# Performance work log

Hardware: AMD Instinct MI355X
Metric: run time of the kernel (lower is better)

The kernel has to match this reference:

```python
import jax, jax.numpy as jnp
import numpy as np

EMBED = 1024
DMODEL = 1024
NHEAD = 16
HEAD = DMODEL // NHEAD  # 64
EPS = 1e-5


def layer_norm(x, g, b):
    mu = jnp.mean(x, axis=-1, keepdims=True)
    var = jnp.var(x, axis=-1, keepdims=True)
    return (x - mu) / jnp.sqrt(var + EPS) * g + b


def setup_inputs() -> dict:
    key = jax.random.key(0)
    ks = jax.random.split(key, 16)
    s = 0.02
    B, T = 2, 2048
    return {
        "x": jax.random.normal(ks[0], (B, T, EMBED), jnp.float32),
        "wq": jax.random.normal(ks[1], (NHEAD, EMBED, HEAD), jnp.float32) * s,
        "bq": jnp.zeros((NHEAD, HEAD), jnp.float32),
        "wk": jax.random.normal(ks[2], (NHEAD, EMBED, HEAD), jnp.float32) * s,
        "bk": jnp.zeros((NHEAD, HEAD), jnp.float32),
        "wv": jax.random.normal(ks[3], (NHEAD, EMBED, HEAD), jnp.float32) * s,
        "bv": jnp.zeros((NHEAD, HEAD), jnp.float32),
        "ln1_g": jnp.ones((EMBED,), jnp.float32),
        "ln1_b": jnp.zeros((EMBED,), jnp.float32),
        "ln2_g": jnp.ones((DMODEL,), jnp.float32),
        "ln2_b": jnp.zeros((DMODEL,), jnp.float32),
        "w1": jax.random.normal(ks[4], (DMODEL, 4 * DMODEL), jnp.float32) * s,
        "b1": jnp.zeros((4 * DMODEL,), jnp.float32),
        "w2": jax.random.normal(ks[5], (4 * DMODEL, EMBED), jnp.float32) * s,
        "b2": jnp.zeros((EMBED,), jnp.float32),
    }


def reference(x, wq, bq, wk, bk, wv, bv, ln1_g, ln1_b, ln2_g, ln2_b, w1, b1, w2, b2):
    B, T, C = x.shape
    h = layer_norm(x, ln1_g, ln1_b)  # note: residual uses the normalized x (as in source)
    # per-head projections, vectorized over heads: [B,H,T,D]
    q = jnp.einsum('btc,hcd->bhtd', h, wq) + bq[None, :, None, :]
    k = jnp.einsum('btc,hcd->bhtd', h, wk) + bk[None, :, None, :]
    v = jnp.einsum('btc,hcd->bhtd', h, wv) + bv[None, :, None, :]
    scores = jnp.einsum('bhtd,bhsd->bhts', q, k) / jnp.sqrt(jnp.float32(HEAD))
    causal = jnp.tril(jnp.ones((T, T), bool))
    scores = jnp.where(causal[None, None], scores, jnp.finfo(scores.dtype).min)
    wei = jax.nn.softmax(scores, axis=-1)
    attn = jnp.einsum('bhts,bhsd->bhtd', wei, v)
    attn = attn.transpose(0, 2, 1, 3).reshape(B, T, NHEAD * HEAD)  # concat heads
    y = h + attn
    z = layer_norm(y, ln2_g, ln2_b)
    ff = jax.nn.relu(z @ w1 + b1) @ w2 + b2
    return z + ff
```

## Files before the change

### kernel.cpp

```cpp
#include <hip/hip_runtime.h>
#include <hip/hip_bf16.h>
#include <cstdint>
#include <cstddef>

typedef __attribute__((ext_vector_type(8))) short bf16x8;
typedef __attribute__((ext_vector_type(4))) float f32x4;
typedef __attribute__((ext_vector_type(4))) short short4v;
typedef __attribute__((ext_vector_type(2))) unsigned int uint2v;

__device__ inline void gload_lds16(const void* g, void* l) {
  __builtin_amdgcn_global_load_lds((const __attribute__((address_space(1))) void*)g,
                                   (__attribute__((address_space(3))) void*)l, 16, 0, 0);
}

__device__ inline float exp2_fast(float x) {
  float r;
  asm volatile("v_exp_f32 %0, %1" : "=v"(r) : "v"(x));
  return r;
}

__device__ inline unsigned int cvt_pk_bf16(float lo, float hi) {
  unsigned int r;
  asm volatile("v_cvt_pk_bf16_f32 %0, %1, %2" : "=v"(r) : "v"(lo), "v"(hi));
  return r;
}

__device__ inline float bf2f(short s) {
  return __uint_as_float(((unsigned int)(unsigned short)s) << 16);
}

__global__ void transpose_pack(const float* __restrict__ src, __hip_bfloat16* __restrict__ dst,
                               int R, int C, int ldDst, long zSrcStride, int zDstRow)
{
  __shared__ float tile[64][65];
  src += (size_t)blockIdx.z * zSrcStride;
  const int r0 = blockIdx.y * 64, c0 = blockIdx.x * 64;
  const int t = threadIdx.x;
#pragma unroll
  for (int i = 0; i < 16; ++i) {
    int idx = i * 256 + t;
    int r = idx >> 6, c = idx & 63;
    tile[r][c] = src[(size_t)(r0 + r) * C + c0 + c];
  }
  __syncthreads();
  const int drow0 = blockIdx.z * zDstRow + c0;
#pragma unroll
  for (int i = 0; i < 16; ++i) {
    int idx = i * 256 + t;
    int cc = idx >> 6, rr = idx & 63;
    dst[(size_t)(drow0 + cc) * ldDst + r0 + rr] = __float2bfloat16(tile[rr][cc]);
  }
}

__global__ void transpose_qkv(const float* __restrict__ wq, const float* __restrict__ wk,
                              const float* __restrict__ wv, __hip_bfloat16* __restrict__ dst)
{
  __shared__ float tile[64][65];
  const int z = blockIdx.z;
  const int seg = z >> 4, h = z & 15;
  const float* src = (seg == 0) ? wq : (seg == 1) ? wk : wv;
  src += (size_t)h * 65536;
  const int r0 = blockIdx.y * 64;
  const int t = threadIdx.x;
#pragma unroll
  for (int i = 0; i < 16; ++i) {
    int idx = i * 256 + t;
    int r = idx >> 6, c = idx & 63;
    tile[r][c] = src[(size_t)(r0 + r) * 64 + c];
  }
  __syncthreads();
  const int drow0 = seg * 1024 + h * 64;
#pragma unroll
  for (int i = 0; i < 16; ++i) {
    int idx = i * 256 + t;
    int cc = idx >> 6, rr = idx & 63;
    dst[(size_t)(drow0 + cc) * 1024 + r0 + rr] = __float2bfloat16(tile[rr][cc]);
  }
}

__global__ void ln_fused(const float* __restrict__ x,
                         const float* __restrict__ g, const float* __restrict__ bta,
                         float* __restrict__ of32, __hip_bfloat16* __restrict__ obf)
{
  const int row = blockIdx.x;
  const int t = threadIdx.x;
  float4 v = ((const float4*)(x + (size_t)row * 1024))[t];
  float s = v.x + v.y + v.z + v.w;
  float ss = v.x * v.x + v.y * v.y + v.z * v.z + v.w * v.w;
#pragma unroll
  for (int off = 1; off < 64; off <<= 1) {
    s += __shfl_xor(s, off);
    ss += __shfl_xor(ss, off);
  }
  __shared__ float sb[4], ssb[4];
  const int w = t >> 6, lane = t & 63;
  if (lane == 0) { sb[w] = s; ssb[w] = ss; }
  __syncthreads();
  s = sb[0] + sb[1] + sb[2] + sb[3];
  ss = ssb[0] + ssb[1] + ssb[2] + ssb[3];
  const float mu = s * (1.f / 1024.f);
  const float var = ss * (1.f / 1024.f) - mu * mu;
  const float rstd = rsqrtf(var + 1e-5f);
  float4 gv = ((const float4*)g)[t];
  float4 bv = ((const float4*)bta)[t];
  float4 o;
  o.x = (v.x - mu) * rstd * gv.x + bv.x;
  o.y = (v.y - mu) * rstd * gv.y + bv.y;
  o.z = (v.z - mu) * rstd * gv.z + bv.z;
  o.w = (v.w - mu) * rstd * gv.w + bv.w;
  ((float4*)(of32 + (size_t)row * 1024))[t] = o;
  __hip_bfloat16 hb[4] = { __float2bfloat16(o.x), __float2bfloat16(o.y),
                           __float2bfloat16(o.z), __float2bfloat16(o.w) };
  *(short4v*)(obf + (size_t)row * 1024 + t * 4) = *(const short4v*)hb;
}

__global__ void ln2_merge_fused(const float* __restrict__ hres,
                                const __hip_bfloat16* __restrict__ Opart,
                                const float* __restrict__ Lpart,
                                const float* __restrict__ g, const float* __restrict__ bta,
                                float* __restrict__ of32, __hip_bfloat16* __restrict__ obf)
{
  const int row = blockIdx.x;
  const int b = row >> 11, tt = row & 2047;
  const int qblk = tt >> 7, qloc = tt & 127;
  const int nch = (qblk >> 2) + 1;
  const int t = threadIdx.x;
  const int hd = t >> 4;
  const int d0 = (t & 15) * 4;
  const int base = ((b * 16 + hd) * 16 + qblk) << 2;

  float4 v = ((const float4*)(hres + (size_t)row * 1024))[t];
  float l = 0.f;
  float o0 = 0.f, o1 = 0.f, o2 = 0.f, o3 = 0.f;
  for (int ch = 0; ch < nch; ++ch) {
    l += Lpart[(size_t)(base + ch) * 128 + qloc];
    short4v o4 = *(const short4v*)(Opart + (size_t)(base + ch) * 8192 + qloc * 64 + d0);
    o0 += bf2f(o4[0]); o1 += bf2f(o4[1]); o2 += bf2f(o4[2]); o3 += bf2f(o4[3]);
  }
  const float inv = 1.f / l;
  v.x += o0 * inv; v.y += o1 * inv; v.z += o2 * inv; v.w += o3 * inv;

  float s = v.x + v.y + v.z + v.w;
  float ss = v.x * v.x + v.y * v.y + v.z * v.z + v.w * v.w;
#pragma unroll
  for (int off = 1; off < 64; off <<= 1) {
    s += __shfl_xor(s, off);
    ss += __shfl_xor(ss, off);
  }
  __shared__ float sb[4], ssb[4];
  const int w = t >> 6, lane = t & 63;
  if (lane == 0) { sb[w] = s; ssb[w] = ss; }
  __syncthreads();
  s = sb[0] + sb[1] + sb[2] + sb[3];
  ss = ssb[0] + ssb[1] + ssb[2] + ssb[3];
  const float mu = s * (1.f / 1024.f);
  const float var = ss * (1.f / 1024.f) - mu * mu;
  const float rstd = rsqrtf(var + 1e-5f);
  float4 gv = ((const float4*)g)[t];
  float4 bv = ((const float4*)bta)[t];
  float4 o;
  o.x = (v.x - mu) * rstd * gv.x + bv.x;
  o.y = (v.y - mu) * rstd * gv.y + bv.y;
  o.z = (v.z - mu) * rstd * gv.z + bv.z;
  o.w = (v.w - mu) * rstd * gv.w + bv.w;
  ((float4*)(of32 + (size_t)row * 1024))[t] = o;
  __hip_bfloat16 hb[4] = { __float2bfloat16(o.x), __float2bfloat16(o.y),
                           __float2bfloat16(o.z), __float2bfloat16(o.w) };
  *(short4v*)(obf + (size_t)row * 1024 + t * 4) = *(const short4v*)hb;
}

template<int EPI>
__global__ __launch_bounds__(512, 2) void gemm_bt(
    const __hip_bfloat16* __restrict__ A, const __hip_bfloat16* __restrict__ Bt,
    int N, int Kf, int kLen,
    const float* __restrict__ bias,
    const float* __restrict__ bq, const float* __restrict__ bk, const float* __restrict__ bv,
    __hip_bfloat16* __restrict__ oq, __hip_bfloat16* __restrict__ ok, __hip_bfloat16* __restrict__ ovt,
    __hip_bfloat16* __restrict__ obf,
    __hip_bfloat16* __restrict__ opart0, __hip_bfloat16* __restrict__ opart1,
    __hip_bfloat16* __restrict__ opart2, __hip_bfloat16* __restrict__ opart3)
{
  __shared__ short As[2][128 * 32];
  __shared__ short Bs[2][256 * 32];
  const int t = threadIdx.x;
  const int lane = t & 63;
  const int w = t >> 6;
  const int wm = w >> 2, wn = w & 3;
  const int l15 = lane & 15, lg = lane >> 4;

  const int nwg = (int)(gridDim.x * gridDim.y);
  int wgid = (int)blockIdx.y * (int)gridDim.x + (int)blockIdx.x;
  wgid = (wgid & 7) * (nwg >> 3) + (wgid >> 3);
  const int bx = wgid % (int)gridDim.x;
  const int by = wgid / (int)gridDim.x;
  const int m0 = by * 128;
  const int n0 = bx * 256;
  const int kBase = (EPI == 2) ? (int)blockIdx.z * kLen : 0;
  const int kEnd0 = kBase + kLen;
  const int kEnd = (kEnd0 > Kf) ? Kf : kEnd0;

  f32x4 acc[4][4];
#pragma unroll
  for (int i = 0; i < 4; ++i)
#pragma unroll
    for (int j = 0; j < 4; ++j)
#pragma unroll
      for (int e = 0; e < 4; ++e) acc[i][j][e] = 0.f;

  auto STAGE = [&](int buf, int kk0) {
    {
      const int r = t >> 2, cc = t & 3;
      const int kk = (cc ^ ((r >> 1) & 3)) * 8;
      gload_lds16(A + (size_t)(m0 + r) * Kf + kk0 + kk, (char*)As + buf * 8192 + t * 16);
    }
#pragma unroll
    for (int i = 0; i < 2; ++i) {
      const int c = t + 512 * i;
      const int r = c >> 2, cc = c & 3;
      const int kk = (cc ^ ((r >> 1) & 3)) * 8;
      gload_lds16(Bt + (size_t)(n0 + r) * Kf + kk0 + kk, (char*)Bs + buf * 16384 + c * 16);
    }
  };

  STAGE(0, kBase);
  int buf = 0;
  for (int k0 = kBase; k0 < kEnd; k0 += 32) {
    const int knext = (k0 + 32 < kEnd) ? k0 + 32 : k0;
    STAGE(buf ^ 1, knext);
    asm volatile("s_waitcnt vmcnt(3)" ::: "memory");
    __builtin_amdgcn_s_barrier();
    asm volatile("" ::: "memory");

    bf16x8 af[4], bfr[4];
#pragma unroll
    for (int fm = 0; fm < 4; ++fm) {
      const int r = wm * 64 + fm * 16 + l15;
      const int kc = lg ^ ((r >> 1) & 3);
      af[fm] = *(const bf16x8*)&As[buf][r * 32 + kc * 8];
    }
#pragma unroll
    for (int fn = 0; fn < 4; ++fn) {
      const int r = wn * 64 + fn * 16 + l15;
      const int kc = lg ^ ((r >> 1) & 3);
      bfr[fn] = *(const bf16x8*)&Bs[buf][r * 32 + kc * 8];
    }
#pragma unroll
    for (int fm = 0; fm < 4; ++fm)
#pragma unroll
      for (int fn = 0; fn < 4; ++fn)
        acc[fm][fn] = __builtin_amdgcn_mfma_f32_16x16x32_bf16(af[fm], bfr[fn], acc[fm][fn], 0, 0, 0);

    asm volatile("" ::: "memory");
    __builtin_amdgcn_s_barrier();
    buf ^= 1;
  }

#pragma unroll
  for (int fm = 0; fm < 4; ++fm) {
    const int mbase = m0 + wm * 64 + fm * 16 + lg * 4;
#pragma unroll
    for (int fn = 0; fn < 4; ++fn) {
      const int n = n0 + wn * 64 + fn * 16 + l15;
      if (EPI == 0) {
        const int seg = n >> 10;
        const int cn = n & 1023;
        const int h = cn >> 6, d = cn & 63;
        const float* bp = (seg == 0) ? bq : (seg == 1) ? bk : bv;
        const float bias_v = bp[cn];
#pragma unroll
        for (int rg = 0; rg < 4; ++rg) {
          const int m = mbase + rg;
          const int b = m >> 11, tt = m & 2047;
          const size_t bh = (size_t)(b * 16 + h);
          const float val = acc[fm][fn][rg] + bias_v;
          if (seg == 0)      oq[(bh * 2048 + tt) * 64 + d] = __float2bfloat16(val);
          else if (seg == 1) ok[(bh * 2048 + tt) * 64 + d] = __float2bfloat16(val);
          else               ovt[(bh * 64 + d) * 2048 + tt] = __float2bfloat16(val);
        }
      } else if (EPI == 1) {
        const float bias_v = bias[n];
#pragma unroll
        for (int rg = 0; rg < 4; ++rg) {
          const int m = mbase + rg;
          float val = acc[fm][fn][rg] + bias_v;
          val = fmaxf(val, 0.f);
          obf[(size_t)m * N + n] = __float2bfloat16(val);
        }
      } else {
        __hip_bfloat16* op = (blockIdx.z == 0) ? opart0 : (blockIdx.z == 1) ? opart1
                           : (blockIdx.z == 2) ? opart2 : opart3;
#pragma unroll
        for (int rg = 0; rg < 4; ++rg) {
          const int m = mbase + rg;
          op[(size_t)m * 1024 + n] = __float2bfloat16(acc[fm][fn][rg]);
        }
      }
    }
  }
}

__global__ void ffn2_merge(const __hip_bfloat16* __restrict__ p0, const __hip_bfloat16* __restrict__ p1,
                           const __hip_bfloat16* __restrict__ p2, const __hip_bfloat16* __restrict__ p3,
                           const float* __restrict__ z, const float* __restrict__ b2,
                           float* __restrict__ out)
{
  const size_t i = ((size_t)blockIdx.x * 256 + threadIdx.x) * 4;
  const float4 c = *(const float4*)(z + i);
  const float4 bb = *(const float4*)(b2 + (i & 1023));
  float o0 = c.x + bb.x, o1 = c.y + bb.y, o2 = c.z + bb.z, o3 = c.w + bb.w;
  short4v a0 = *(const short4v*)(p0 + i);
  short4v a1 = *(const short4v*)(p1 + i);
  short4v a2 = *(const short4v*)(p2 + i);
  short4v a3 = *(const short4v*)(p3 + i);
  o0 += bf2f(a0[0]) + bf2f(a1[0]) + bf2f(a2[0]) + bf2f(a3[0]);
  o1 += bf2f(a0[1]) + bf2f(a1[1]) + bf2f(a2[1]) + bf2f(a3[1]);
  o2 += bf2f(a0[2]) + bf2f(a1[2]) + bf2f(a2[2]) + bf2f(a3[2]);
  o3 += bf2f(a0[3]) + bf2f(a1[3]) + bf2f(a2[3]) + bf2f(a3[3]);
  float4 o; o.x = o0; o.y = o1; o.z = o2; o.w = o3;
  *(float4*)(out + i) = o;
}

__global__ __launch_bounds__(256, 3) void flash_attn(
    const __hip_bfloat16* __restrict__ Q, const __hip_bfloat16* __restrict__ Kb,
    const __hip_bfloat16* __restrict__ Vt,
    __hip_bfloat16* __restrict__ Opart, float* __restrict__ Lpart)
{
  __shared__ short Ks[2][64 * 64];
  __shared__ short Vs[2][64 * 64];
  __shared__ short P2[4][32 * 72];
  const int t = threadIdx.x;
  const int lane = t & 63, w = t >> 6;
  const int l15 = lane & 15, lg = lane >> 4;
  const int chunk = blockIdx.x, bh = blockIdx.z;
  const int qblk = 15 - (int)blockIdx.y;
  const int q0 = qblk * 128;
  const int s_base = chunk * 512;
  if (s_base > q0 + 127) return;
  const int s_hi = (s_base + 512 < q0 + 128) ? s_base + 512 : q0 + 128;
  const int ntiles = (s_hi - s_base) >> 6;
  const int qw = q0 + w * 32;

  const __hip_bfloat16* Qbh = Q + (size_t)bh * 2048 * 64;
  const __hip_bfloat16* Kbh = Kb + (size_t)bh * 2048 * 64;
  const __hip_bfloat16* Vbh = Vt + (size_t)bh * 64 * 2048;

  bf16x8 qf[2][2];
#pragma unroll
  for (int fm = 0; fm < 2; ++fm)
#pragma unroll
    for (int kc = 0; kc < 2; ++kc)
      qf[fm][kc] = *(const bf16x8*)(Qbh + (size_t)(qw + fm * 16 + l15) * 64 + kc * 32 + lg * 8);

  const int srow = (w << 4) + (lane >> 3);
  const int schunk = ((lane & 7) ^ (lane >> 3)) * 8;

  auto STAGE = [&](int bufi, int s0) {
#pragma unroll
    for (int i = 0; i < 2; ++i) {
      const int r = srow + i * 8;
      const int dst = bufi * 8192 + w * 2048 + i * 1024 + lane * 16;
      gload_lds16(Kbh + (size_t)(s0 + r) * 64 + schunk, (char*)Ks + dst);
      gload_lds16(Vbh + (size_t)r * 2048 + s0 + schunk, (char*)Vs + dst);
    }
  };

  f32x4 o_acc[2][4];
  float lpart[2] = {0.f, 0.f};
#pragma unroll
  for (int fm = 0; fm < 2; ++fm)
#pragma unroll
    for (int fd = 0; fd < 4; ++fd)
#pragma unroll
      for (int e = 0; e < 4; ++e) o_acc[fm][fd][e] = 0.f;

  const float C = 0.18033688011112042f;

  STAGE(0, s_base);
  int cur = 0;
  for (int ti = 0; ti < ntiles; ++ti) {
    const int s0 = s_base + ti * 64;
    const int nxt = (ti + 1 < ntiles) ? s0 + 64 : s0;
    STAGE(cur ^ 1, nxt);
    asm volatile("s_waitcnt vmcnt(4)" ::: "memory");
    __builtin_amdgcn_s_barrier();
    asm volatile("" ::: "memory");

    if (s0 <= qw + 31) {
      f32x4 s_acc[2][4];
#pragma unroll
      for (int fm = 0; fm < 2; ++fm)
#pragma unroll
        for (int fn = 0; fn < 4; ++fn)
#pragma unroll
          for (int e = 0; e < 4; ++e) s_acc[fm][fn][e] = 0.f;
      __builtin_amdgcn_s_setprio(1);
#pragma unroll
      for (int kc = 0; kc < 2; ++kc)
#pragma unroll
        for (int fn = 0; fn < 4; ++fn) {
          const int r = fn * 16 + l15;
          bf16x8 kf = *(const bf16x8*)&Ks[cur][r * 64 + ((((kc << 2) | lg) ^ (l15 & 7)) << 3)];
          s_acc[0][fn] = __builtin_amdgcn_mfma_f32_16x16x32_bf16(kf, qf[0][kc], s_acc[0][fn], 0, 0, 0);
          s_acc[1][fn] = __builtin_amdgcn_mfma_f32_16x16x32_bf16(kf, qf[1][kc], s_acc[1][fn], 0, 0, 0);
        }
      __builtin_amdgcn_s_setprio(0);

      const bool needmask = (s0 + 63 > qw);
      float pr[2][4][4];
#pragma unroll
      for (int fm = 0; fm < 2; ++fm) {
        const int qv = qw + fm * 16 + l15;
#pragma unroll
        for (int fn = 0; fn < 4; ++fn)
#pragma unroll
          for (int rg = 0; rg < 4; ++rg) {
            float p = exp2_fast(s_acc[fm][fn][rg] * C);
            if (needmask) {
              const int sg = s0 + fn * 16 + lg * 4 + rg;
              p = (sg <= qv) ? p : 0.f;
            }
            pr[fm][fn][rg] = p;
            lpart[fm] += p;
          }
      }

#pragma unroll
      for (int fm = 0; fm < 2; ++fm)
#pragma unroll
        for (int fn = 0; fn < 4; ++fn) {
          uint2v u;
          u.x = cvt_pk_bf16(pr[fm][fn][0], pr[fm][fn][1]);
          u.y = cvt_pk_bf16(pr[fm][fn][2], pr[fm][fn][3]);
          *(uint2v*)&P2[w][(fm * 16 + l15) * 72 + fn * 16 + lg * 4] = u;
        }

      __builtin_amdgcn_s_setprio(1);
#pragma unroll
      for (int kc = 0; kc < 2; ++kc) {
        bf16x8 pf0 = *(const bf16x8*)&P2[w][(l15) * 72 + kc * 32 + lg * 8];
        bf16x8 pf1 = *(const bf16x8*)&P2[w][(16 + l15) * 72 + kc * 32 + lg * 8];
#pragma unroll
        for (int fd = 0; fd < 4; ++fd) {
          const int r = fd * 16 + l15;
          bf16x8 vf = *(const bf16x8*)&Vs[cur][r * 64 + ((((kc << 2) | lg) ^ (l15 & 7)) << 3)];
          o_acc[0][fd] = __builtin_amdgcn_mfma_f32_16x16x32_bf16(vf, pf0, o_acc[0][fd], 0, 0, 0);
          o_acc[1][fd] = __builtin_amdgcn_mfma_f32_16x16x32_bf16(vf, pf1, o_acc[1][fd], 0, 0, 0);
        }
      }
      __builtin_amdgcn_s_setprio(0);
    }

    asm volatile("" ::: "memory");
    __builtin_amdgcn_s_barrier();
    cur ^= 1;
  }

  const int pslot = ((bh * 16 + qblk) << 2) + chunk;
  __hip_bfloat16* op = Opart + (size_t)pslot * 8192;
#pragma unroll
  for (int fm = 0; fm < 2; ++fm) {
    float l = lpart[fm];
    l += __shfl_xor(l, 16);
    l += __shfl_xor(l, 32);
    const int qloc = w * 32 + fm * 16 + l15;
    if (lg == 0) Lpart[pslot * 128 + qloc] = l;
#pragma unroll
    for (int fd = 0; fd < 4; ++fd) {
      uint2v u;
      u.x = cvt_pk_bf16(o_acc[fm][fd][0], o_acc[fm][fd][1]);
      u.y = cvt_pk_bf16(o_acc[fm][fd][2], o_acc[fm][fd][3]);
      *(uint2v*)(op + (size_t)qloc * 64 + fd * 16 + lg * 4) = u;
    }
  }
}

extern "C" void kernel_launch(void* const* d_in, const int* in_sizes, int n_in,
                              void* d_out, int out_size, void* d_ws, size_t ws_size,
                              hipStream_t stream) {
  const float* x    = (const float*)d_in[0];
  const float* wq   = (const float*)d_in[1];
  const float* bq   = (const float*)d_in[2];
  const float* wk   = (const float*)d_in[3];
  const float* bk   = (const float*)d_in[4];
  const float* wv   = (const float*)d_in[5];
  const float* bv   = (const float*)d_in[6];
  const float* ln1g = (const float*)d_in[7];
  const float* ln1b = (const float*)d_in[8];
  const float* ln2g = (const float*)d_in[9];
  const float* ln2b = (const float*)d_in[10];
  const float* w1   = (const float*)d_in[11];
  const float* b1   = (const float*)d_in[12];
  const float* w2   = (const float*)d_in[13];
  const float* b2   = (const float*)d_in[14];
  float* out = (float*)d_out;

  char* ws = (char*)d_ws;
  const size_t MB = 1024 * 1024;
  __hip_bfloat16* h_bf  = (__hip_bfloat16*)(ws + 0);
  float* z_f32          = (float*)(ws + 0);
  __hip_bfloat16* qb    = (__hip_bfloat16*)(ws + 8 * MB);
  __hip_bfloat16* kb    = (__hip_bfloat16*)(ws + 16 * MB);
  __hip_bfloat16* z_bf  = (__hip_bfloat16*)(ws + 16 * MB);
  __hip_bfloat16* vtb   = (__hip_bfloat16*)(ws + 24 * MB);
  __hip_bfloat16* ff1   = (__hip_bfloat16*)(ws + 24 * MB);
  float* h_f32          = (float*)(ws + 32 * MB);
  __hip_bfloat16* p3    = (__hip_bfloat16*)(ws + 32 * MB);
  __hip_bfloat16* Opart = (__hip_bfloat16*)(ws + 48 * MB);
  __hip_bfloat16* p0    = (__hip_bfloat16*)(ws + 56 * MB);
  __hip_bfloat16* p1    = (__hip_bfloat16*)(ws + 64 * MB);
  __hip_bfloat16* p2    = (__hip_bfloat16*)(ws + 72 * MB);
  float* Lpart          = (float*)(ws + 80 * MB);
  __hip_bfloat16* wqkvT = (__hip_bfloat16*)(ws + 88 * MB);
  __hip_bfloat16* w1T   = (__hip_bfloat16*)(ws + 96 * MB);
  __hip_bfloat16* w2T   = (__hip_bfloat16*)(ws + 104 * MB);

  transpose_qkv<<<dim3(1, 16, 48), 256, 0, stream>>>(wq, wk, wv, wqkvT);
  transpose_pack<<<dim3(64, 16, 1), 256, 0, stream>>>(w1, w1T, 1024, 4096, 1024, 0, 0);
  transpose_pack<<<dim3(16, 64, 1), 256, 0, stream>>>(w2, w2T, 4096, 1024, 4096, 0, 0);

  ln_fused<<<4096, 256, 0, stream>>>(x, ln1g, ln1b, h_f32, h_bf);

  gemm_bt<0><<<dim3(12, 32), 512, 0, stream>>>(h_bf, wqkvT, 3072, 1024, 1024,
      nullptr, bq, bk, bv, qb, kb, vtb, nullptr, nullptr, nullptr, nullptr, nullptr);

  flash_attn<<<dim3(4, 16, 32), 256, 0, stream>>>(qb, kb, vtb, Opart, Lpart);

  ln2_merge_fused<<<4096, 256, 0, stream>>>(h_f32, Opart, Lpart, ln2g, ln2b, z_f32, z_bf);

  gemm_bt<1><<<dim3(16, 32), 512, 0, stream>>>(z_bf, w1T, 4096, 1024, 1024,
      b1, nullptr, nullptr, nullptr, nullptr, nullptr, nullptr, ff1, nullptr, nullptr, nullptr, nullptr);

  gemm_bt<2><<<dim3(4, 32, 4), 512, 0, stream>>>(ff1, w2T, 1024, 4096, 1024,
      nullptr, nullptr, nullptr, nullptr, nullptr, nullptr, nullptr, nullptr, p0, p1, p2, p3);

  ffn2_merge<<<4096, 256, 0, stream>>>(p0, p1, p2, p3, z_f32, b2, out);
}
```

Measured before the change: 229.2 us.

## Split flash attention across 8 waves with 16 query rows per wave

The flash attention block goes from 4 to 8 waves, and each wave now handles 16 query rows instead of 32. Every thread issues one K and one V async load per tile instead of two, and the wait count is adjusted to match. The aim is to raise wave-level parallelism and hide latency better, and to let the causal skip work at a finer grain. In exchange each wave reuses every K/V fragment read from LDS for half as many MFMAs, which doubles LDS read traffic per FLOP, and barrier cost grows with more waves.

```diff
diff --git a/kernel.cpp b/kernel.cpp
--- a/kernel.cpp
+++ b/kernel.cpp
@@ -320,14 +320,14 @@
   *(float4*)(out + i) = o;
 }
 
-__global__ __launch_bounds__(256, 3) void flash_attn(
+__global__ __launch_bounds__(512, 3) void flash_attn(
     const __hip_bfloat16* __restrict__ Q, const __hip_bfloat16* __restrict__ Kb,
     const __hip_bfloat16* __restrict__ Vt,
     __hip_bfloat16* __restrict__ Opart, float* __restrict__ Lpart)
 {
   __shared__ short Ks[2][64 * 64];
   __shared__ short Vs[2][64 * 64];
-  __shared__ short P2[4][32 * 72];
+  __shared__ short P2[8][16 * 72];
   const int t = threadIdx.x;
   const int lane = t & 63, w = t >> 6;
   const int l15 = lane & 15, lg = lane >> 4;
@@ -338,40 +338,32 @@
   if (s_base > q0 + 127) return;
   const int s_hi = (s_base + 512 < q0 + 128) ? s_base + 512 : q0 + 128;
   const int ntiles = (s_hi - s_base) >> 6;
-  const int qw = q0 + w * 32;
+  const int qw = q0 + w * 16;
 
   const __hip_bfloat16* Qbh = Q + (size_t)bh * 2048 * 64;
   const __hip_bfloat16* Kbh = Kb + (size_t)bh * 2048 * 64;
   const __hip_bfloat16* Vbh = Vt + (size_t)bh * 64 * 2048;
 
-  bf16x8 qf[2][2];
-#pragma unroll
-  for (int fm = 0; fm < 2; ++fm)
-#pragma unroll
-    for (int kc = 0; kc < 2; ++kc)
-      qf[fm][kc] = *(const bf16x8*)(Qbh + (size_t)(qw + fm * 16 + l15) * 64 + kc * 32 + lg * 8);
-
-  const int srow = (w << 4) + (lane >> 3);
-  const int schunk = ((lane & 7) ^ (lane >> 3)) * 8;
+  bf16x8 qf[2];
+#pragma unroll
+  for (int kc = 0; kc < 2; ++kc)
+    qf[kc] = *(const bf16x8*)(Qbh + (size_t)(qw + l15) * 64 + kc * 32 + lg * 8);
+
+  const int srow = t >> 3;
+  const int schunk = ((t & 7) ^ (srow & 7)) * 8;
 
   auto STAGE = [&](int bufi, int s0) {
-#pragma unroll
-    for (int i = 0; i < 2; ++i) {
-      const int r = srow + i * 8;
-      const int dst = bufi * 8192 + w * 2048 + i * 1024 + lane * 16;
-      gload_lds16(Kbh + (size_t)(s0 + r) * 64 + schunk, (char*)Ks + dst);
-      gload_lds16(Vbh + (size_t)r * 2048 + s0 + schunk, (char*)Vs + dst);
-    }
+    const int dst = bufi * 8192 + t * 16;
+    gload_lds16(Kbh + (size_t)(s0 + srow) * 64 + schunk, (char*)Ks + dst);
+    gload_lds16(Vbh + (size_t)srow * 2048 + s0 + schunk, (char*)Vs + dst);
   };
 
-  f32x4 o_acc[2][4];
-  float lpart[2] = {0.f, 0.f};
-#pragma unroll
-  for (int fm = 0; fm < 2; ++fm)
-#pragma unroll
-    for (int fd = 0; fd < 4; ++fd)
-#pragma unroll
-      for (int e = 0; e < 4; ++e) o_acc[fm][fd][e] = 0.f;
+  f32x4 o_acc[4];
+  float lpart = 0.f;
+#pragma unroll
+  for (int fd = 0; fd < 4; ++fd)
+#pragma unroll
+    for (int e = 0; e < 4; ++e) o_acc[fd][e] = 0.f;
 
   const float C = 0.18033688011112042f;
 
@@ -381,18 +373,16 @@
     const int s0 = s_base + ti * 64;
     const int nxt = (ti + 1 < ntiles) ? s0 + 64 : s0;
     STAGE(cur ^ 1, nxt);
-    asm volatile("s_waitcnt vmcnt(4)" ::: "memory");
+    asm volatile("s_waitcnt vmcnt(2)" ::: "memory");
     __builtin_amdgcn_s_barrier();
     asm volatile("" ::: "memory");
 
-    if (s0 <= qw + 31) {
-      f32x4 s_acc[2][4];
-#pragma unroll
-      for (int fm = 0; fm < 2; ++fm)
-#pragma unroll
-        for (int fn = 0; fn < 4; ++fn)
-#pragma unroll
-          for (int e = 0; e < 4; ++e) s_acc[fm][fn][e] = 0.f;
+    if (s0 <= qw + 15) {
+      f32x4 s_acc[4];
+#pragma unroll
+      for (int fn = 0; fn < 4; ++fn)
+#pragma unroll
+        for (int e = 0; e < 4; ++e) s_acc[fn][e] = 0.f;
       __builtin_amdgcn_s_setprio(1);
 #pragma unroll
       for (int kc = 0; kc < 2; ++kc)
@@ -400,51 +390,40 @@
         for (int fn = 0; fn < 4; ++fn) {
           const int r = fn * 16 + l15;
           bf16x8 kf = *(const bf16x8*)&Ks[cur][r * 64 + ((((kc << 2) | lg) ^ (l15 & 7)) << 3)];
-          s_acc[0][fn] = __builtin_amdgcn_mfma_f32_16x16x32_bf16(kf, qf[0][kc], s_acc[0][fn], 0, 0, 0);
-          s_acc[1][fn] = __builtin_amdgcn_mfma_f32_16x16x32_bf16(kf, qf[1][kc], s_acc[1][fn], 0, 0, 0);
+          s_acc[fn] = __builtin_amdgcn_mfma_f32_16x16x32_bf16(kf, qf[kc], s_acc[fn], 0, 0, 0);
         }
       __builtin_amdgcn_s_setprio(0);
 
       const bool needmask = (s0 + 63 > qw);
-      float pr[2][4][4];
-#pragma unroll
-      for (int fm = 0; fm < 2; ++fm) {
-        const int qv = qw + fm * 16 + l15;
-#pragma unroll
-        for (int fn = 0; fn < 4; ++fn)
-#pragma unroll
-          for (int rg = 0; rg < 4; ++rg) {
-            float p = exp2_fast(s_acc[fm][fn][rg] * C);
-            if (needmask) {
-              const int sg = s0 + fn * 16 + lg * 4 + rg;
-              p = (sg <= qv) ? p : 0.f;
-            }
-            pr[fm][fn][rg] = p;
-            lpart[fm] += p;
+      const int qv = qw + l15;
+#pragma unroll
+      for (int fn = 0; fn < 4; ++fn) {
+        float p[4];
+#pragma unroll
+        for (int rg = 0; rg < 4; ++rg) {
+          float pv = exp2_fast(s_acc[fn][rg] * C);
+          if (needmask) {
+            const int sg = s0 + fn * 16 + lg * 4 + rg;
+            pv = (sg <= qv) ? pv : 0.f;
           }
+          p[rg] = pv;
+          lpart += pv;
+        }
+        uint2v u;
+        u.x = cvt_pk_bf16(p[0], p[1]);
+        u.y = cvt_pk_bf16(p[2], p[3]);
+        *(uint2v*)&P2[w][l15 * 72 + fn * 16 + lg * 4] = u;
       }
 
-#pragma unroll
-      for (int fm = 0; fm < 2; ++fm)
-#pragma unroll
-        for (int fn = 0; fn < 4; ++fn) {
-          uint2v u;
-          u.x = cvt_pk_bf16(pr[fm][fn][0], pr[fm][fn][1]);
-          u.y = cvt_pk_bf16(pr[fm][fn][2], pr[fm][fn][3]);
-          *(uint2v*)&P2[w][(fm * 16 + l15) * 72 + fn * 16 + lg * 4] = u;
-        }
-
       __builtin_amdgcn_s_setprio(1);
 #pragma unroll
       for (int kc = 0; kc < 2; ++kc) {
-        bf16x8 pf0 = *(const bf16x8*)&P2[w][(l15) * 72 + kc * 32 + lg * 8];
-        bf16x8 pf1 = *(const bf16x8*)&P2[w][(16 + l15) * 72 + kc * 32 + lg * 8];
+        bf16x8 pf = *(const bf16x8*)&P2[w][l15 * 72 + kc * 32 + lg * 8];
 #pragma unroll
         for (int fd = 0; fd < 4; ++fd) {
           const int r = fd * 16 + l15;
           bf16x8 vf = *(const bf16x8*)&Vs[cur][r * 64 + ((((kc << 2) | lg) ^ (l15 & 7)) << 3)];
-          o_acc[0][fd] = __builtin_amdgcn_mfma_f32_16x16x32_bf16(vf, pf0, o_acc[0][fd], 0, 0, 0);
-          o_acc[1][fd] = __builtin_amdgcn_mfma_f32_16x16x32_bf16(vf, pf1, o_acc[1][fd], 0, 0, 0);
+          o_acc[fd] = __builtin_amdgcn_mfma_f32_16x16x32_bf16(vf, pf, o_acc[fd], 0, 0, 0);
         }
       }
       __builtin_amdgcn_s_setprio(0);
@@ -457,18 +436,17 @@
 
   const int pslot = ((bh * 16 + qblk) << 2) + chunk;
   __hip_bfloat16* op = Opart + (size_t)pslot * 8192;
-#pragma unroll
-  for (int fm = 0; fm < 2; ++fm) {
-    float l = lpart[fm];
+  {
+    float l = lpart;
     l += __shfl_xor(l, 16);
     l += __shfl_xor(l, 32);
-    const int qloc = w * 32 + fm * 16 + l15;
+    const int qloc = w * 16 + l15;
     if (lg == 0) Lpart[pslot * 128 + qloc] = l;
 #pragma unroll
     for (int fd = 0; fd < 4; ++fd) {
       uint2v u;
-      u.x = cvt_pk_bf16(o_acc[fm][fd][0], o_acc[fm][fd][1]);
-      u.y = cvt_pk_bf16(o_acc[fm][fd][2], o_acc[fm][fd][3]);
+      u.x = cvt_pk_bf16(o_acc[fd][0], o_acc[fd][1]);
+      u.y = cvt_pk_bf16(o_acc[fd][2], o_acc[fd][3]);
       *(uint2v*)(op + (size_t)qloc * 64 + fd * 16 + lg * 4) = u;
     }
   }
@@ -523,7 +501,7 @@
   gemm_bt<0><<<dim3(12, 32), 512, 0, stream>>>(h_bf, wqkvT, 3072, 1024, 1024,
       nullptr, bq, bk, bv, qb, kb, vtb, nullptr, nullptr, nullptr, nullptr, nullptr);
 
-  flash_attn<<<dim3(4, 16, 32), 256, 0, stream>>>(qb, kb, vtb, Opart, Lpart);
+  flash_attn<<<dim3(4, 16, 32), 512, 0, stream>>>(qb, kb, vtb, Opart, Lpart);
 
   ln2_merge_fused<<<4096, 256, 0, stream>>>(h_f32, Opart, Lpart, ln2g, ln2b, z_f32, z_bf);
 
```

New measurement: 226.4 us. About the same (-1.2%).
